# Kernel optimization log

Measured on AMD Instinct MI355X. Metric: run time of the kernel, lower is better.

Reference implementation:

```python
import jax, jax.numpy as jnp
import numpy as np

D = 1024      # model_dim
H = 2048      # expert hidden_dim
E = 8         # num routed experts
TOP_K = 2
N_SHARED = 1
B, S = 2, 1024


def setup_inputs() -> dict:
    key = jax.random.key(0)
    ks = jax.random.split(key, 12)
    sc = 0.02
    return {
        "hidden": jax.random.normal(ks[0], (B, S, D), jnp.float32),
        # router Linear(D -> E); stored as [in, out]
        "router_w": jax.random.normal(ks[1], (D, E), jnp.float32) * sc,
        "router_b": jnp.zeros((E,), jnp.float32),
        # shared expert (1): Linear(D->H), Linear(H->D)
        "sw1": jax.random.normal(ks[2], (D, H), jnp.float32) * sc,
        "sb1": jnp.zeros((H,), jnp.float32),
        "sw2": jax.random.normal(ks[3], (H, D), jnp.float32) * sc,
        "sb2": jnp.zeros((D,), jnp.float32),
        # routed experts, stacked over E
        "rw1": jax.random.normal(ks[4], (E, D, H), jnp.float32) * sc,
        "rb1": jnp.zeros((E, H), jnp.float32),
        "rw2": jax.random.normal(ks[5], (E, H, D), jnp.float32) * sc,
        "rb2": jnp.zeros((E, D), jnp.float32),
    }


def reference(hidden, router_w, router_b, sw1, sb1, sw2, sb2, rw1, rb1, rw2, rb2):
    b, s, d = hidden.shape
    T = b * s
    flat = hidden.reshape(T, d)                              # [T, D]

    # --- router ---
    router_logits = flat @ router_w + router_b               # [T, E]
    router_probs = jax.nn.softmax(router_logits, axis=-1)
    topk_probs, topk_idx = jax.lax.top_k(router_probs, TOP_K)  # [T, K]

    # per-(token, expert) mixing weight: sum of top-k probs that hit expert e
    weights = jnp.zeros_like(router_probs).at[
        jnp.arange(T)[:, None], topk_idx
    ].add(topk_probs)                                        # [T, E]

    # --- shared expert(s) (1 expert -> mean == itself) ---
    sh = jax.nn.gelu(flat @ sw1 + sb1, approximate=False)    # [T, H]
    shared_out = (sh @ sw2 + sb2) / N_SHARED                 # [T, D]

    # --- routed experts: dense all-expert eval weighted by routing weights ---
    # (identical math to the gather/FFN/index_add loop: weight is 0 for
    #  tokens not routed to expert e)
    h1 = jax.nn.gelu(jnp.einsum('td,edh->teh', flat, rw1) + rb1[None],
                     approximate=False)                      # [T, E, H]
    expert_out = jnp.einsum('teh,ehd->ted', h1, rw2) + rb2[None]  # [T, E, D]
    mixed = jnp.einsum('ted,te->td', expert_out, weights)    # [T, D]

    return (shared_out + mixed).reshape(b, s, d)
```

## Files before the change

### kernel.cpp

```cpp
#include <hip/hip_runtime.h>
#include <hip/hip_bf16.h>

#define T_TOK 2048
#define DDIM  1024
#define HDIM  2048
#define NEXP  8
#define NSEG  9

typedef unsigned short u16;
typedef __attribute__((ext_vector_type(4))) float f32x4;
typedef __attribute__((ext_vector_type(8))) short bf16x8;
typedef __attribute__((ext_vector_type(4))) unsigned short u16x4;

__device__ __forceinline__ u16 f2bf(float x) {
  union { float f; unsigned int u; } v; v.f = x;
  unsigned int r = v.u + 0x7fffu + ((v.u >> 16) & 1u);
  return (u16)(r >> 16);
}
__device__ __forceinline__ float gelu_exact(float x) {
  return 0.5f * x * (1.0f + erff(x * 0.70710678118654752f));
}
__device__ __forceinline__ int swz4(int row) {
  return (row & 3) ^ ((row >> 2) & 3);
}

__device__ __forceinline__ void gload16(const void* g, void* l) {
  __builtin_amdgcn_global_load_lds(
      (const __attribute__((address_space(1))) unsigned int*)g,
      (__attribute__((address_space(3))) unsigned int*)l, 16, 0, 0);
}

__global__ __launch_bounds__(256) void router_kernel(
    const float* __restrict__ x, const float* __restrict__ rw,
    const float* __restrict__ rb, u16* __restrict__ xb,
    float* __restrict__ weights, int* __restrict__ counts,
    int* __restrict__ lists)
{
  int wv = threadIdx.x >> 6, lane = threadIdx.x & 63;
  int t = blockIdx.x * 4 + wv;
  const float* xrow = x + (size_t)t * DDIM;
  float acc[NEXP];
#pragma unroll
  for (int e = 0; e < NEXP; e++) acc[e] = 0.f;
#pragma unroll
  for (int i = 0; i < 4; i++) {
    int d0 = i * 256 + lane * 4;
    f32x4 xv = *(const f32x4*)(xrow + d0);
    u16x4 pk;
#pragma unroll
    for (int j = 0; j < 4; j++) {
      float xs = xv[j];
      pk[j] = f2bf(xs);
      const float* wr = rw + (size_t)(d0 + j) * NEXP;
#pragma unroll
      for (int e = 0; e < NEXP; e++) acc[e] = fmaf(xs, wr[e], acc[e]);
    }
    *(u16x4*)(xb + (size_t)t * DDIM + d0) = pk;
  }
#pragma unroll
  for (int off = 32; off >= 1; off >>= 1)
#pragma unroll
    for (int e = 0; e < NEXP; e++) acc[e] += __shfl_xor(acc[e], off);

  if (lane == 0) {
    float lg[NEXP], mx = -1e30f;
#pragma unroll
    for (int e = 0; e < NEXP; e++) { lg[e] = acc[e] + rb[e]; mx = fmaxf(mx, lg[e]); }
    float p[NEXP], s = 0.f;
#pragma unroll
    for (int e = 0; e < NEXP; e++) { p[e] = expf(lg[e] - mx); s += p[e]; }
    float inv = 1.0f / s;
#pragma unroll
    for (int e = 0; e < NEXP; e++) p[e] *= inv;
    int i1 = 0;
#pragma unroll
    for (int e = 1; e < NEXP; e++) if (p[e] > p[i1]) i1 = e;
    int i2 = (i1 == 0) ? 1 : 0;
#pragma unroll
    for (int e = 0; e < NEXP; e++) if (e != i1 && p[e] > p[i2]) i2 = e;
#pragma unroll
    for (int e = 0; e < NEXP; e++)
      weights[(size_t)t * NEXP + e] = (e == i1) ? p[i1] : (e == i2) ? p[i2] : 0.f;
    int p1 = atomicAdd(counts + i1, 1); lists[i1 * T_TOK + p1] = t;
    int p2 = atomicAdd(counts + i2, 1); lists[i2 * T_TOK + p2] = t;
    lists[NEXP * T_TOK + t] = t;
  }
}

__global__ void seg_kernel(int* counts, int* segoff, int* ytab, int* nyt) {
  counts[NEXP] = T_TOK;
  int off = 0, n = 0;
  for (int e = 0; e < NSEG; e++) {
    segoff[e] = off;
    int c = counts[e];
    for (int my = 0; my * 128 < c; my++) ytab[n++] = e * 256 + my;
    off += c;
  }
  *nyt = n;
}

__global__ __launch_bounds__(256) void transpose_bf16_kernel(
    const float* __restrict__ rin, const float* __restrict__ sin_,
    u16* __restrict__ rout, u16* __restrict__ sout, int R, int C)
{
  __shared__ float tile[32][33];
  int b = blockIdx.z;
  const float* inb = (b < NEXP) ? rin + (size_t)b * R * C : sin_;
  u16* outb = (b < NEXP) ? rout + (size_t)b * R * C : sout;
  int r0 = blockIdx.y * 32, c0 = blockIdx.x * 32;
  int tx = threadIdx.x & 31, ty = threadIdx.x >> 5;
#pragma unroll
  for (int j = 0; j < 4; j++) {
    int r = ty + j * 8;
    tile[r][tx] = inb[(size_t)(r0 + r) * C + c0 + tx];
  }
  __syncthreads();
#pragma unroll
  for (int j = 0; j < 4; j++) {
    int rr = ty + j * 8;
    outb[(size_t)(c0 + rr) * R + r0 + tx] = f2bf(tile[tx][rr]);
  }
}


__global__ __launch_bounds__(256) void gemm1_kernel(
    const u16* __restrict__ Xb, const u16* __restrict__ rw1t,
    const u16* __restrict__ sw1t, const float* __restrict__ rb1,
    const float* __restrict__ sb1, const int* __restrict__ counts,
    const int* __restrict__ segoff, const int* __restrict__ lists,
    const int* __restrict__ ytab, const int* __restrict__ nyt,
    u16* __restrict__ H1)
{
  __shared__ u16 Alds[3][128 * 32];
  __shared__ u16 Blds[3][128 * 32];

  int tid = threadIdx.x, lane = tid & 63;
  int wv = tid >> 6, wm = wv >> 1, wn = wv & 1;
  int kc = lane >> 4, lr = lane & 15;

  int srow[2], soff[2];
#pragma unroll
  for (int r = 0; r < 2; r++) {
    int i = r * 256 + tid;
    srow[r] = i >> 2;
    soff[r] = (((i & 3) ^ swz4(i >> 2)) * 8);
  }
  int aoff[4], boff[4];
#pragma unroll
  for (int f = 0; f < 4; f++) {
    int ra = wm * 64 + f * 16 + lr;
    int rb_ = wn * 64 + f * 16 + lr;
    aoff[f] = ra * 32 + ((kc ^ swz4(ra)) * 8);
    boff[f] = rb_ * 32 + ((kc ^ swz4(rb_)) * 8);
  }

  int ntile = nyt[0] * (HDIM / 128);
  for (int t = blockIdx.x; t < ntile; t += gridDim.x) {
    int yt = t >> 4, nx = t & 15;
    int em = ytab[yt];
    int e = em >> 8, m0 = (em & 255) * 128, n0 = nx * 128;
    int cnt = counts[e];
    const u16* Bt = (e < NEXP) ? (rw1t + (size_t)e * HDIM * DDIM) : sw1t;
    const float* bias = (e < NEXP) ? (rb1 + (size_t)e * HDIM) : sb1;
    const int* list = lists + e * T_TOK;
    int seg = segoff[e];

    size_t abase[2], bbase[2];
#pragma unroll
    for (int r = 0; r < 2; r++) {
      int tok = list[min(m0 + srow[r], cnt - 1)];
      abase[r] = (size_t)tok * DDIM + soff[r];
      bbase[r] = (size_t)(n0 + srow[r]) * DDIM + soff[r];
    }

    f32x4 acc[4][4];
#pragma unroll
    for (int i = 0; i < 4; i++)
#pragma unroll
      for (int j = 0; j < 4; j++) acc[i][j] = (f32x4){0.f, 0.f, 0.f, 0.f};

#pragma unroll
    for (int r = 0; r < 2; r++) {
      int i = r * 256 + tid;
      gload16(Xb + abase[r], &Alds[0][i * 8]);
      gload16(Bt + bbase[r], &Blds[0][i * 8]);
    }

    const int NS = DDIM / 32;
    int cur = 0;
    for (int s = 0; s < NS; s++) {
      int nxt = cur + 1; if (nxt == 3) nxt = 0;
      if (s + 1 < NS) {
        int kk = (s + 1) * 32;
        u16* Ad = &Alds[nxt][0];
        u16* Bd = &Blds[nxt][0];
#pragma unroll
        for (int r = 0; r < 2; r++) {
          int i = r * 256 + tid;
          gload16(Xb + abase[r] + kk, Ad + i * 8);
          gload16(Bt + bbase[r] + kk, Bd + i * 8);
        }
        asm volatile("s_waitcnt vmcnt(4)" ::: "memory");
      } else {
        asm volatile("s_waitcnt vmcnt(0)" ::: "memory");
      }
      __builtin_amdgcn_s_barrier();
      __builtin_amdgcn_sched_barrier(0);

      const u16* Ac = &Alds[cur][0];
      const u16* Bc = &Blds[cur][0];
      bf16x8 af[4], bfr[4];
#pragma unroll
      for (int f = 0; f < 4; f++) {
        af[f]  = *(const bf16x8*)(Ac + aoff[f]);
        bfr[f] = *(const bf16x8*)(Bc + boff[f]);
      }
#pragma unroll
      for (int mf = 0; mf < 4; mf++)
#pragma unroll
        for (int nf = 0; nf < 4; nf++)
          acc[mf][nf] = __builtin_amdgcn_mfma_f32_16x16x32_bf16(af[mf], bfr[nf], acc[mf][nf], 0, 0, 0);
      cur = nxt;
    }

#pragma unroll
    for (int nf = 0; nf < 4; nf++) {
      int col = n0 + wn * 64 + nf * 16 + lr;
      float b = bias[col];
#pragma unroll
      for (int mf = 0; mf < 4; mf++) {
#pragma unroll
        for (int rg = 0; rg < 4; rg++) {
          int mt = wm * 64 + mf * 16 + kc * 4 + rg;
          if (m0 + mt < cnt) {
            float v = acc[mf][nf][rg] + b;
            H1[(size_t)(seg + m0 + mt) * HDIM + col] = f2bf(gelu_exact(v));
          }
        }
      }
    }
    __builtin_amdgcn_s_barrier();
    __builtin_amdgcn_sched_barrier(0);
  }
}

__global__ __launch_bounds__(256) void gemm2_kernel(
    const u16* __restrict__ H1, const u16* __restrict__ rw2t,
    const u16* __restrict__ sw2t, const float* __restrict__ rb2,
    const float* __restrict__ sb2, const float* __restrict__ weights,
    const int* __restrict__ counts, const int* __restrict__ segoff,
    const int* __restrict__ lists, const int* __restrict__ ytab,
    const int* __restrict__ nyt, float* __restrict__ out)
{
  __shared__ u16 Alds[3][128 * 32];
  __shared__ u16 Blds[3][128 * 32];

  int tid = threadIdx.x, lane = tid & 63;
  int wv = tid >> 6, wm = wv >> 1, wn = wv & 1;
  int kc = lane >> 4, lr = lane & 15;

  int srow[2], soff[2];
#pragma unroll
  for (int r = 0; r < 2; r++) {
    int i = r * 256 + tid;
    srow[r] = i >> 2;
    soff[r] = (((i & 3) ^ swz4(i >> 2)) * 8);
  }
  int aoff[4], boff[4];
#pragma unroll
  for (int f = 0; f < 4; f++) {
    int ra = wm * 64 + f * 16 + lr;
    int rb_ = wn * 64 + f * 16 + lr;
    aoff[f] = ra * 32 + ((kc ^ swz4(ra)) * 8);
    boff[f] = rb_ * 32 + ((kc ^ swz4(rb_)) * 8);
  }

  int ntile = nyt[0] * (DDIM / 128) * 2;
  for (int t = blockIdx.x; t < ntile; t += gridDim.x) {
    int kh = t & 1, nx = (t >> 1) & 7, yt = t >> 4;
    int em = ytab[yt];
    int e = em >> 8, m0 = (em & 255) * 128, n0 = nx * 128;
    int cnt = counts[e];
    const u16* Bt = (e < NEXP) ? (rw2t + (size_t)e * DDIM * HDIM) : sw2t;
    const float* bias = (e < NEXP) ? (rb2 + (size_t)e * DDIM) : sb2;
    const int* list = lists + e * T_TOK;
    int seg = segoff[e];
    int k0 = kh * 1024;

    size_t abase[2], bbase[2];
#pragma unroll
    for (int r = 0; r < 2; r++) {
      abase[r] = (size_t)(seg + min(m0 + srow[r], cnt - 1)) * HDIM + k0 + soff[r];
      bbase[r] = (size_t)(n0 + srow[r]) * HDIM + k0 + soff[r];
    }

    f32x4 acc[4][4];
#pragma unroll
    for (int i = 0; i < 4; i++)
#pragma unroll
      for (int j = 0; j < 4; j++) acc[i][j] = (f32x4){0.f, 0.f, 0.f, 0.f};

#pragma unroll
    for (int r = 0; r < 2; r++) {
      int i = r * 256 + tid;
      gload16(H1 + abase[r], &Alds[0][i * 8]);
      gload16(Bt + bbase[r], &Blds[0][i * 8]);
    }

    const int NS = 1024 / 32;
    int cur = 0;
    for (int s = 0; s < NS; s++) {
      int nxt = cur + 1; if (nxt == 3) nxt = 0;
      if (s + 1 < NS) {
        int kk = (s + 1) * 32;
        u16* Ad = &Alds[nxt][0];
        u16* Bd = &Blds[nxt][0];
#pragma unroll
        for (int r = 0; r < 2; r++) {
          int i = r * 256 + tid;
          gload16(H1 + abase[r] + kk, Ad + i * 8);
          gload16(Bt + bbase[r] + kk, Bd + i * 8);
        }
        asm volatile("s_waitcnt vmcnt(4)" ::: "memory");
      } else {
        asm volatile("s_waitcnt vmcnt(0)" ::: "memory");
      }
      __builtin_amdgcn_s_barrier();
      __builtin_amdgcn_sched_barrier(0);

      const u16* Ac = &Alds[cur][0];
      const u16* Bc = &Blds[cur][0];
      bf16x8 af[4], bfr[4];
#pragma unroll
      for (int f = 0; f < 4; f++) {
        af[f]  = *(const bf16x8*)(Ac + aoff[f]);
        bfr[f] = *(const bf16x8*)(Bc + boff[f]);
      }
#pragma unroll
      for (int mf = 0; mf < 4; mf++)
#pragma unroll
        for (int nf = 0; nf < 4; nf++)
          acc[mf][nf] = __builtin_amdgcn_mfma_f32_16x16x32_bf16(af[mf], bfr[nf], acc[mf][nf], 0, 0, 0);
      cur = nxt;
    }

    float biasv[4];
#pragma unroll
    for (int nf = 0; nf < 4; nf++)
      biasv[nf] = (kh == 0) ? bias[n0 + wn * 64 + nf * 16 + lr] : 0.f;

#pragma unroll
    for (int mf = 0; mf < 4; mf++) {
#pragma unroll
      for (int rg = 0; rg < 4; rg++) {
        int mt = wm * 64 + mf * 16 + kc * 4 + rg;
        int mrow = m0 + mt;
        if (mrow < cnt) {
          int tok = list[mrow];
          float w = (e < NEXP) ? weights[(size_t)tok * NEXP + e] : 1.0f;
          float* orow = out + (size_t)tok * DDIM + n0 + wn * 64 + lr;
#pragma unroll
          for (int nf = 0; nf < 4; nf++)
            atomicAdd(orow + nf * 16, w * (acc[mf][nf][rg] + biasv[nf]));
        }
      }
    }
    __builtin_amdgcn_s_barrier();
    __builtin_amdgcn_sched_barrier(0);
  }
}

extern "C" void kernel_launch(void* const* d_in, const int* in_sizes, int n_in,
                              void* d_out, int out_size, void* d_ws, size_t ws_size,
                              hipStream_t stream) {
  (void)in_sizes; (void)n_in; (void)out_size; (void)ws_size;
  const float* hidden   = (const float*)d_in[0];
  const float* router_w = (const float*)d_in[1];
  const float* router_b = (const float*)d_in[2];
  const float* sw1 = (const float*)d_in[3];
  const float* sb1 = (const float*)d_in[4];
  const float* sw2 = (const float*)d_in[5];
  const float* sb2 = (const float*)d_in[6];
  const float* rw1 = (const float*)d_in[7];
  const float* rb1 = (const float*)d_in[8];
  const float* rw2 = (const float*)d_in[9];
  const float* rb2 = (const float*)d_in[10];
  float* out = (float*)d_out;

  char* ws = (char*)d_ws;
  u16* Xb      = (u16*)(ws + 0);
  u16* rw1t    = (u16*)(ws + 4194304);
  u16* rw2t    = (u16*)(ws + 37748736);
  u16* sw1t    = (u16*)(ws + 71303168);
  u16* sw2t    = (u16*)(ws + 75497472);
  u16* H1      = (u16*)(ws + 79691776);
  float* weights = (float*)(ws + 104857600);
  int* counts  = (int*)(ws + 104923136);
  int* segoff  = (int*)(ws + 104923200);
  int* lists   = (int*)(ws + 104923264);
  int* ytab    = (int*)(ws + 104996992);
  int* nyt     = (int*)(ws + 104997632);

  hipMemsetAsync(counts, 0, 64, stream);
  hipMemsetAsync(out, 0, (size_t)T_TOK * DDIM * sizeof(float), stream);

  router_kernel<<<T_TOK / 4, 256, 0, stream>>>(hidden, router_w, router_b, Xb,
                                               weights, counts, lists);
  seg_kernel<<<1, 1, 0, stream>>>(counts, segoff, ytab, nyt);

  transpose_bf16_kernel<<<dim3(HDIM / 32, DDIM / 32, NSEG), 256, 0, stream>>>(
      rw1, sw1, rw1t, sw1t, DDIM, HDIM);
  transpose_bf16_kernel<<<dim3(DDIM / 32, HDIM / 32, NSEG), 256, 0, stream>>>(
      rw2, sw2, rw2t, sw2t, HDIM, DDIM);

  gemm1_kernel<<<1024, 256, 0, stream>>>(
      Xb, rw1t, sw1t, rb1, sb1, counts, segoff, lists, ytab, nyt, H1);
  gemm2_kernel<<<1024, 256, 0, stream>>>(
      H1, rw2t, sw2t, rb2, sb2, weights, counts, segoff, lists, ytab, nyt, out);
}
```

Before: 274.8 us.

## Fuse weight transpose and bf16 conversion into GEMM B-tile loading

Removes the two separate transpose/convert kernels that turned all fp32 expert weights into transposed bf16 copies. Each GEMM instead loads fp32 weights straight from the original layout into registers, converts them to bf16, and writes them transposed into a swizzled, double-buffered LDS tile one stage ahead. It also raises wave priority around the MFMA block. The trade-off is that every GEMM tile now reads fp32 weights (twice the bytes) and does the conversion repeatedly across M tiles, in exchange for skipping a full weight-sized transpose pass and its extra write.

```diff
diff --git a/kernel.cpp b/kernel.cpp
--- a/kernel.cpp
+++ b/kernel.cpp
@@ -99,44 +99,22 @@
   *nyt = n;
 }
 
-__global__ __launch_bounds__(256) void transpose_bf16_kernel(
-    const float* __restrict__ rin, const float* __restrict__ sin_,
-    u16* __restrict__ rout, u16* __restrict__ sout, int R, int C)
-{
-  __shared__ float tile[32][33];
-  int b = blockIdx.z;
-  const float* inb = (b < NEXP) ? rin + (size_t)b * R * C : sin_;
-  u16* outb = (b < NEXP) ? rout + (size_t)b * R * C : sout;
-  int r0 = blockIdx.y * 32, c0 = blockIdx.x * 32;
-  int tx = threadIdx.x & 31, ty = threadIdx.x >> 5;
-#pragma unroll
-  for (int j = 0; j < 4; j++) {
-    int r = ty + j * 8;
-    tile[r][tx] = inb[(size_t)(r0 + r) * C + c0 + tx];
-  }
-  __syncthreads();
-#pragma unroll
-  for (int j = 0; j < 4; j++) {
-    int rr = ty + j * 8;
-    outb[(size_t)(c0 + rr) * R + r0 + tx] = f2bf(tile[tx][rr]);
-  }
-}
-
 
 __global__ __launch_bounds__(256) void gemm1_kernel(
-    const u16* __restrict__ Xb, const u16* __restrict__ rw1t,
-    const u16* __restrict__ sw1t, const float* __restrict__ rb1,
+    const u16* __restrict__ Xb, const float* __restrict__ rw1,
+    const float* __restrict__ sw1, const float* __restrict__ rb1,
     const float* __restrict__ sb1, const int* __restrict__ counts,
     const int* __restrict__ segoff, const int* __restrict__ lists,
     const int* __restrict__ ytab, const int* __restrict__ nyt,
     u16* __restrict__ H1)
 {
   __shared__ u16 Alds[3][128 * 32];
-  __shared__ u16 Blds[3][128 * 32];
+  __shared__ u16 Blds[2][128 * 32];
 
   int tid = threadIdx.x, lane = tid & 63;
   int wv = tid >> 6, wm = wv >> 1, wn = wv & 1;
   int kc = lane >> 4, lr = lane & 15;
+  int hi = lane >> 5, nln = (lane & 31) * 4;
 
   int srow[2], soff[2];
 #pragma unroll
@@ -153,6 +131,10 @@
     aoff[f] = ra * 32 + ((kc ^ swz4(ra)) * 8);
     boff[f] = rb_ * 32 + ((kc ^ swz4(rb_)) * 8);
   }
+  int bw[4];
+#pragma unroll
+  for (int j = 0; j < 4; j++)
+    bw[j] = (nln + j) * 32 + ((wv ^ j ^ (lane & 3)) << 3) + hi * 4;
 
   int ntile = nyt[0] * (HDIM / 128);
   for (int t = blockIdx.x; t < ntile; t += gridDim.x) {
@@ -160,18 +142,18 @@
     int em = ytab[yt];
     int e = em >> 8, m0 = (em & 255) * 128, n0 = nx * 128;
     int cnt = counts[e];
-    const u16* Bt = (e < NEXP) ? (rw1t + (size_t)e * HDIM * DDIM) : sw1t;
+    const float* Wf = (e < NEXP) ? (rw1 + (size_t)e * DDIM * HDIM) : sw1;
     const float* bias = (e < NEXP) ? (rb1 + (size_t)e * HDIM) : sb1;
     const int* list = lists + e * T_TOK;
     int seg = segoff[e];
 
-    size_t abase[2], bbase[2];
+    size_t abase[2];
 #pragma unroll
     for (int r = 0; r < 2; r++) {
       int tok = list[min(m0 + srow[r], cnt - 1)];
       abase[r] = (size_t)tok * DDIM + soff[r];
-      bbase[r] = (size_t)(n0 + srow[r]) * DDIM + soff[r];
-    }
+    }
+    const float* Wbp = Wf + (size_t)(wv * 8 + hi * 4) * HDIM + n0 + nln;
 
     f32x4 acc[4][4];
 #pragma unroll
@@ -179,48 +161,81 @@
 #pragma unroll
       for (int j = 0; j < 4; j++) acc[i][j] = (f32x4){0.f, 0.f, 0.f, 0.f};
 
-#pragma unroll
-    for (int r = 0; r < 2; r++) {
-      int i = r * 256 + tid;
-      gload16(Xb + abase[r], &Alds[0][i * 8]);
-      gload16(Bt + bbase[r], &Blds[0][i * 8]);
-    }
-
     const int NS = DDIM / 32;
-    int cur = 0;
+    f32x4 vBa, vBb, vBc, vBd;
+    vBa = *(const f32x4*)(Wbp);
+    vBb = *(const f32x4*)(Wbp + HDIM);
+    vBc = *(const f32x4*)(Wbp + 2 * HDIM);
+    vBd = *(const f32x4*)(Wbp + 3 * HDIM);
+#pragma unroll
+    for (int r = 0; r < 2; r++)
+      gload16(Xb + abase[r], &Alds[0][(r * 256 + tid) * 8]);
+    {
+      u16* Bd = &Blds[0][0];
+#pragma unroll
+      for (int j = 0; j < 4; j++) {
+        u16x4 pk;
+        pk[0] = f2bf(vBa[j]); pk[1] = f2bf(vBb[j]);
+        pk[2] = f2bf(vBc[j]); pk[3] = f2bf(vBd[j]);
+        *(u16x4*)(Bd + bw[j]) = pk;
+      }
+    }
+    {
+      const float* Wk = Wbp + (size_t)32 * HDIM;
+      vBa = *(const f32x4*)(Wk);
+      vBb = *(const f32x4*)(Wk + HDIM);
+      vBc = *(const f32x4*)(Wk + 2 * HDIM);
+      vBd = *(const f32x4*)(Wk + 3 * HDIM);
+    }
+
     for (int s = 0; s < NS; s++) {
-      int nxt = cur + 1; if (nxt == 3) nxt = 0;
       if (s + 1 < NS) {
         int kk = (s + 1) * 32;
-        u16* Ad = &Alds[nxt][0];
-        u16* Bd = &Blds[nxt][0];
-#pragma unroll
-        for (int r = 0; r < 2; r++) {
-          int i = r * 256 + tid;
-          gload16(Xb + abase[r] + kk, Ad + i * 8);
-          gload16(Bt + bbase[r] + kk, Bd + i * 8);
-        }
-        asm volatile("s_waitcnt vmcnt(4)" ::: "memory");
+        int nb = s + 1; nb = (nb >= 3) ? (nb % 3) : nb;
+#pragma unroll
+        for (int r = 0; r < 2; r++)
+          gload16(Xb + abase[r] + kk, &Alds[nb][(r * 256 + tid) * 8]);
+        asm volatile("s_waitcnt vmcnt(6)" ::: "memory");
       } else {
         asm volatile("s_waitcnt vmcnt(0)" ::: "memory");
       }
+      asm volatile("s_waitcnt lgkmcnt(0)" ::: "memory");
       __builtin_amdgcn_s_barrier();
       __builtin_amdgcn_sched_barrier(0);
 
-      const u16* Ac = &Alds[cur][0];
-      const u16* Bc = &Blds[cur][0];
+      if (s + 1 < NS) {
+        u16* Bd = &Blds[(s + 1) & 1][0];
+#pragma unroll
+        for (int j = 0; j < 4; j++) {
+          u16x4 pk;
+          pk[0] = f2bf(vBa[j]); pk[1] = f2bf(vBb[j]);
+          pk[2] = f2bf(vBc[j]); pk[3] = f2bf(vBd[j]);
+          *(u16x4*)(Bd + bw[j]) = pk;
+        }
+        if (s + 2 < NS) {
+          const float* Wk = Wbp + (size_t)((s + 2) * 32) * HDIM;
+          vBa = *(const f32x4*)(Wk);
+          vBb = *(const f32x4*)(Wk + HDIM);
+          vBc = *(const f32x4*)(Wk + 2 * HDIM);
+          vBd = *(const f32x4*)(Wk + 3 * HDIM);
+        }
+      }
+
+      const u16* Ac = &Alds[s % 3][0];
+      const u16* Bc = &Blds[s & 1][0];
       bf16x8 af[4], bfr[4];
 #pragma unroll
       for (int f = 0; f < 4; f++) {
         af[f]  = *(const bf16x8*)(Ac + aoff[f]);
         bfr[f] = *(const bf16x8*)(Bc + boff[f]);
       }
+      __builtin_amdgcn_s_setprio(1);
 #pragma unroll
       for (int mf = 0; mf < 4; mf++)
 #pragma unroll
         for (int nf = 0; nf < 4; nf++)
           acc[mf][nf] = __builtin_amdgcn_mfma_f32_16x16x32_bf16(af[mf], bfr[nf], acc[mf][nf], 0, 0, 0);
-      cur = nxt;
+      __builtin_amdgcn_s_setprio(0);
     }
 
 #pragma unroll
@@ -245,19 +260,20 @@
 }
 
 __global__ __launch_bounds__(256) void gemm2_kernel(
-    const u16* __restrict__ H1, const u16* __restrict__ rw2t,
-    const u16* __restrict__ sw2t, const float* __restrict__ rb2,
+    const u16* __restrict__ H1, const float* __restrict__ rw2,
+    const float* __restrict__ sw2, const float* __restrict__ rb2,
     const float* __restrict__ sb2, const float* __restrict__ weights,
     const int* __restrict__ counts, const int* __restrict__ segoff,
     const int* __restrict__ lists, const int* __restrict__ ytab,
     const int* __restrict__ nyt, float* __restrict__ out)
 {
   __shared__ u16 Alds[3][128 * 32];
-  __shared__ u16 Blds[3][128 * 32];
+  __shared__ u16 Blds[2][128 * 32];
 
   int tid = threadIdx.x, lane = tid & 63;
   int wv = tid >> 6, wm = wv >> 1, wn = wv & 1;
   int kc = lane >> 4, lr = lane & 15;
+  int hi = lane >> 5, nln = (lane & 31) * 4;
 
   int srow[2], soff[2];
 #pragma unroll
@@ -274,6 +290,10 @@
     aoff[f] = ra * 32 + ((kc ^ swz4(ra)) * 8);
     boff[f] = rb_ * 32 + ((kc ^ swz4(rb_)) * 8);
   }
+  int bw[4];
+#pragma unroll
+  for (int j = 0; j < 4; j++)
+    bw[j] = (nln + j) * 32 + ((wv ^ j ^ (lane & 3)) << 3) + hi * 4;
 
   int ntile = nyt[0] * (DDIM / 128) * 2;
   for (int t = blockIdx.x; t < ntile; t += gridDim.x) {
@@ -281,18 +301,17 @@
     int em = ytab[yt];
     int e = em >> 8, m0 = (em & 255) * 128, n0 = nx * 128;
     int cnt = counts[e];
-    const u16* Bt = (e < NEXP) ? (rw2t + (size_t)e * DDIM * HDIM) : sw2t;
+    const float* Wf = (e < NEXP) ? (rw2 + (size_t)e * HDIM * DDIM) : sw2;
     const float* bias = (e < NEXP) ? (rb2 + (size_t)e * DDIM) : sb2;
     const int* list = lists + e * T_TOK;
     int seg = segoff[e];
     int k0 = kh * 1024;
 
-    size_t abase[2], bbase[2];
-#pragma unroll
-    for (int r = 0; r < 2; r++) {
+    size_t abase[2];
+#pragma unroll
+    for (int r = 0; r < 2; r++)
       abase[r] = (size_t)(seg + min(m0 + srow[r], cnt - 1)) * HDIM + k0 + soff[r];
-      bbase[r] = (size_t)(n0 + srow[r]) * HDIM + k0 + soff[r];
-    }
+    const float* Wbp = Wf + (size_t)(k0 + wv * 8 + hi * 4) * DDIM + n0 + nln;
 
     f32x4 acc[4][4];
 #pragma unroll
@@ -300,48 +319,81 @@
 #pragma unroll
       for (int j = 0; j < 4; j++) acc[i][j] = (f32x4){0.f, 0.f, 0.f, 0.f};
 
-#pragma unroll
-    for (int r = 0; r < 2; r++) {
-      int i = r * 256 + tid;
-      gload16(H1 + abase[r], &Alds[0][i * 8]);
-      gload16(Bt + bbase[r], &Blds[0][i * 8]);
-    }
-
     const int NS = 1024 / 32;
-    int cur = 0;
+    f32x4 vBa, vBb, vBc, vBd;
+    vBa = *(const f32x4*)(Wbp);
+    vBb = *(const f32x4*)(Wbp + DDIM);
+    vBc = *(const f32x4*)(Wbp + 2 * DDIM);
+    vBd = *(const f32x4*)(Wbp + 3 * DDIM);
+#pragma unroll
+    for (int r = 0; r < 2; r++)
+      gload16(H1 + abase[r], &Alds[0][(r * 256 + tid) * 8]);
+    {
+      u16* Bd = &Blds[0][0];
+#pragma unroll
+      for (int j = 0; j < 4; j++) {
+        u16x4 pk;
+        pk[0] = f2bf(vBa[j]); pk[1] = f2bf(vBb[j]);
+        pk[2] = f2bf(vBc[j]); pk[3] = f2bf(vBd[j]);
+        *(u16x4*)(Bd + bw[j]) = pk;
+      }
+    }
+    {
+      const float* Wk = Wbp + (size_t)32 * DDIM;
+      vBa = *(const f32x4*)(Wk);
+      vBb = *(const f32x4*)(Wk + DDIM);
+      vBc = *(const f32x4*)(Wk + 2 * DDIM);
+      vBd = *(const f32x4*)(Wk + 3 * DDIM);
+    }
+
     for (int s = 0; s < NS; s++) {
-      int nxt = cur + 1; if (nxt == 3) nxt = 0;
       if (s + 1 < NS) {
         int kk = (s + 1) * 32;
-        u16* Ad = &Alds[nxt][0];
-        u16* Bd = &Blds[nxt][0];
-#pragma unroll
-        for (int r = 0; r < 2; r++) {
-          int i = r * 256 + tid;
-          gload16(H1 + abase[r] + kk, Ad + i * 8);
-          gload16(Bt + bbase[r] + kk, Bd + i * 8);
-        }
-        asm volatile("s_waitcnt vmcnt(4)" ::: "memory");
+        int nb = s + 1; nb = (nb >= 3) ? (nb % 3) : nb;
+#pragma unroll
+        for (int r = 0; r < 2; r++)
+          gload16(H1 + abase[r] + kk, &Alds[nb][(r * 256 + tid) * 8]);
+        asm volatile("s_waitcnt vmcnt(6)" ::: "memory");
       } else {
         asm volatile("s_waitcnt vmcnt(0)" ::: "memory");
       }
+      asm volatile("s_waitcnt lgkmcnt(0)" ::: "memory");
       __builtin_amdgcn_s_barrier();
       __builtin_amdgcn_sched_barrier(0);
 
-      const u16* Ac = &Alds[cur][0];
-      const u16* Bc = &Blds[cur][0];
+      if (s + 1 < NS) {
+        u16* Bd = &Blds[(s + 1) & 1][0];
+#pragma unroll
+        for (int j = 0; j < 4; j++) {
+          u16x4 pk;
+          pk[0] = f2bf(vBa[j]); pk[1] = f2bf(vBb[j]);
+          pk[2] = f2bf(vBc[j]); pk[3] = f2bf(vBd[j]);
+          *(u16x4*)(Bd + bw[j]) = pk;
+        }
+        if (s + 2 < NS) {
+          const float* Wk = Wbp + (size_t)((s + 2) * 32) * DDIM;
+          vBa = *(const f32x4*)(Wk);
+          vBb = *(const f32x4*)(Wk + DDIM);
+          vBc = *(const f32x4*)(Wk + 2 * DDIM);
+          vBd = *(const f32x4*)(Wk + 3 * DDIM);
+        }
+      }
+
+      const u16* Ac = &Alds[s % 3][0];
+      const u16* Bc = &Blds[s & 1][0];
       bf16x8 af[4], bfr[4];
 #pragma unroll
       for (int f = 0; f < 4; f++) {
         af[f]  = *(const bf16x8*)(Ac + aoff[f]);
         bfr[f] = *(const bf16x8*)(Bc + boff[f]);
       }
+      __builtin_amdgcn_s_setprio(1);
 #pragma unroll
       for (int mf = 0; mf < 4; mf++)
 #pragma unroll
         for (int nf = 0; nf < 4; nf++)
           acc[mf][nf] = __builtin_amdgcn_mfma_f32_16x16x32_bf16(af[mf], bfr[nf], acc[mf][nf], 0, 0, 0);
-      cur = nxt;
+      __builtin_amdgcn_s_setprio(0);
     }
 
     float biasv[4];
@@ -389,17 +441,13 @@
 
   char* ws = (char*)d_ws;
   u16* Xb      = (u16*)(ws + 0);
-  u16* rw1t    = (u16*)(ws + 4194304);
-  u16* rw2t    = (u16*)(ws + 37748736);
-  u16* sw1t    = (u16*)(ws + 71303168);
-  u16* sw2t    = (u16*)(ws + 75497472);
-  u16* H1      = (u16*)(ws + 79691776);
-  float* weights = (float*)(ws + 104857600);
-  int* counts  = (int*)(ws + 104923136);
-  int* segoff  = (int*)(ws + 104923200);
-  int* lists   = (int*)(ws + 104923264);
-  int* ytab    = (int*)(ws + 104996992);
-  int* nyt     = (int*)(ws + 104997632);
+  u16* H1      = (u16*)(ws + 4194304);
+  float* weights = (float*)(ws + 29360128);
+  int* counts  = (int*)(ws + 29425664);
+  int* segoff  = (int*)(ws + 29425728);
+  int* lists   = (int*)(ws + 29425792);
+  int* ytab    = (int*)(ws + 29499520);
+  int* nyt     = (int*)(ws + 29500160);
 
   hipMemsetAsync(counts, 0, 64, stream);
   hipMemsetAsync(out, 0, (size_t)T_TOK * DDIM * sizeof(float), stream);
@@ -408,13 +456,8 @@
                                                weights, counts, lists);
   seg_kernel<<<1, 1, 0, stream>>>(counts, segoff, ytab, nyt);
 
-  transpose_bf16_kernel<<<dim3(HDIM / 32, DDIM / 32, NSEG), 256, 0, stream>>>(
-      rw1, sw1, rw1t, sw1t, DDIM, HDIM);
-  transpose_bf16_kernel<<<dim3(DDIM / 32, HDIM / 32, NSEG), 256, 0, stream>>>(
-      rw2, sw2, rw2t, sw2t, HDIM, DDIM);
-
   gemm1_kernel<<<1024, 256, 0, stream>>>(
-      Xb, rw1t, sw1t, rb1, sb1, counts, segoff, lists, ytab, nyt, H1);
+      Xb, rw1, sw1, rb1, sb1, counts, segoff, lists, ytab, nyt, H1);
   gemm2_kernel<<<1024, 256, 0, stream>>>(
-      H1, rw2t, sw2t, rb2, sb2, weights, counts, segoff, lists, ytab, nyt, out);
-}
+      H1, rw2, sw2, rb2, sb2, weights, counts, segoff, lists, ytab, nyt, out);
+}
```

After: 255.8 us. 1.07x faster.
